# Optimization experiments

Hardware: AMD Instinct MI355X
Metric: run time of the kernel (lower is better)

The kernel has to match this reference:

```python
import jax, jax.numpy as jnp
import numpy as np
from jax import lax

NUM_CLASSES = 80
TOPK = 13
ALPHA = 1.0
BETA = 6.0
EPS = 1e-9
P = 150000
N = 256


def _make_boxes(key, n, scale):
    k1, k2 = jax.random.split(key)
    xy = jax.random.uniform(k1, (n, 2), dtype=jnp.float32) * scale
    wh = jax.random.uniform(k2, (n, 2), dtype=jnp.float32) * (0.2 * scale) + 1.0
    return jnp.concatenate([xy, xy + wh], axis=-1)  # valid x1y1x2y2


def setup_inputs() -> dict:
    key = jax.random.key(0)
    k1, k2, k3, k4 = jax.random.split(key, 4)
    cls_pred = jax.random.uniform(k1, (P, NUM_CLASSES), dtype=jnp.float32)
    bbox_pred = _make_boxes(k2, P, 640.0)
    bbox_gt = _make_boxes(k3, N, 640.0)
    # FG labels are > 0 (code indexes cls_pred[label-1])
    label_gt = jax.random.randint(k4, (N, 1), 1, NUM_CLASSES + 1, dtype=jnp.int32)
    return {"cls_pred": cls_pred, "bbox_pred": bbox_pred, "label_gt": label_gt, "bbox_gt": bbox_gt}


def _ious(bbox1, bbox2, eps=EPS):
    # bbox1: (N,4) gt, bbox2: (P,4) pred -> (N,P)
    b1 = bbox1[:, None, :]
    b2 = bbox2[None, :, :]
    x1y1 = jnp.maximum(b1[..., 0:2], b2[..., 0:2])
    x2y2 = jnp.minimum(b1[..., 2:4], b2[..., 2:4])
    inter = jnp.clip(x2y2 - x1y1, 0.0).prod(-1)
    area1 = jnp.clip(b1[..., 2:4] - b1[..., 0:2], 0.0).prod(-1)
    area2 = jnp.clip(b2[..., 2:4] - b2[..., 0:2], 0.0).prod(-1)
    return inter / (area1 + area2 - inter + eps)


def _metrics_topk(metrics, topk, eps=EPS):
    n, num_priors = metrics.shape
    topk_vals, topk_idxs = lax.top_k(metrics, topk)  # (N,k)
    keep = topk_vals.max(axis=-1, keepdims=True) > eps
    topk_idxs = jnp.where(keep, topk_idxs, 0)
    rows = jnp.arange(n)[:, None]
    counts = jnp.zeros((n, num_priors), jnp.int32).at[rows, topk_idxs].add(1)
    is_in_topk = jnp.where(counts > 1, 0, counts)
    return is_in_topk.astype(metrics.dtype)


def reference(cls_pred, bbox_pred, label_gt, bbox_gt):
    num_priors, num_classes = cls_pred.shape
    n_gt = bbox_gt.shape[0]
    ious = _ious(bbox_gt, bbox_pred)  # (N,P)
    lbl = label_gt.reshape(-1).astype(jnp.int32)  # (N,)
    bbox_cls_scores = jnp.take(cls_pred.T, lbl - 1, axis=0)  # (N,P)
    alignment_metrics = jnp.power(bbox_cls_scores, ALPHA) * jnp.power(ious, BETA)
    mask_positive = _metrics_topk(alignment_metrics, TOPK)  # (N,P) float 0/1
    mask_positive_sum = mask_positive.sum(axis=0)  # (P,)
    # conflict resolution: priors claimed by >1 gt go to the max-iou gt.
    # Applying unconditionally equals the torch data-dependent branch.
    is_max_iou = (jnp.arange(n_gt)[:, None] == ious.argmax(axis=0)[None, :]).astype(ious.dtype)
    mask_positive = jnp.where(mask_positive_sum[None, :] > 1, is_max_iou, mask_positive)
    mask_positive_sum = mask_positive.sum(axis=0)
    assigned_gt_index = mask_positive.argmax(axis=0)  # (P,)
    assigned_labels = lbl[assigned_gt_index]  # (P,)
    assigned_cls = jax.nn.one_hot(assigned_labels - 1, num_classes, dtype=jnp.int32)
    assigned_bboxes = bbox_gt[assigned_gt_index]  # (P,4)
    assigned_labels = jnp.where(mask_positive_sum > 0, assigned_labels, 0)
    return (assigned_gt_index, assigned_labels, assigned_cls, assigned_bboxes)
```

## Files before the change

### kernel.cpp

```cpp
#include <hip/hip_runtime.h>

#define TOPK 13
#define NCLS 80
#define EPSF 1e-9f
#define NSEG 32
#define GPB  8
#define CAP3 512

typedef unsigned long long u64;
typedef float __attribute__((ext_vector_type(4))) f32x4;

__device__ __forceinline__ u64 shfl_xor64(u64 x, int m) {
    int lo = __shfl_xor((int)(unsigned)(x & 0xFFFFFFFFull), m, 64);
    int hi = __shfl_xor((int)(unsigned)(x >> 32), m, 64);
    return ((u64)(unsigned)hi << 32) | (unsigned)lo;
}
__device__ __forceinline__ u64 shfl64(u64 x, int src) {
    int lo = __shfl((int)(unsigned)(x & 0xFFFFFFFFull), src, 64);
    int hi = __shfl((int)(unsigned)(x >> 32), src, 64);
    return ((u64)(unsigned)hi << 32) | (unsigned)lo;
}

__global__ __launch_bounds__(256) void setup(const int* __restrict__ lbl,
                                             int* __restrict__ count,
                                             int* __restrict__ firstg,
                                             int* __restrict__ gorder, int P, int N) {
    int t = threadIdx.x;
    if (blockIdx.x == 0) {
        __shared__ int key[256];
        key[t] = (t < N) ? ((lbl[t] << 8) | t) : 0x7FFFFFFF;
        __syncthreads();
        for (int k = 2; k <= 256; k <<= 1) {
            for (int j = k >> 1; j >= 1; j >>= 1) {
                int ixj = t ^ j;
                if (ixj > t) {
                    int a = key[t], b = key[ixj];
                    bool up = ((t & k) == 0);
                    if (up ? (a > b) : (a < b)) { key[t] = b; key[ixj] = a; }
                }
                __syncthreads();
            }
        }
        if (t < N) gorder[t] = key[t] & 0xFF;
    } else {
        int base = (blockIdx.x - 1) * 1024 + t * 4;
        if (base + 3 < P) {
            *(int4*)&count[base]  = make_int4(0, 0, 0, 0);
            *(int4*)&firstg[base] = make_int4(0x7FFFFFFF, 0x7FFFFFFF, 0x7FFFFFFF, 0x7FFFFFFF);
        } else {
            for (int i = base; i < P; i++) { count[i] = 0; firstg[i] = 0x7FFFFFFF; }
        }
    }
}

__global__ __launch_bounds__(512, 8) void phaseA1(const float* __restrict__ cls,
                                                  const float4* __restrict__ bboxp,
                                                  const float4* __restrict__ bboxg,
                                                  const int* __restrict__ lbl,
                                                  const int* __restrict__ gorder,
                                                  u64* __restrict__ cand,
                                                  int* __restrict__ cnt,
                                                  int P, int N, int seglen) {
#pragma clang fp contract(off)
    const int s = blockIdx.x, tile = blockIdx.y, t = threadIdx.x;
    const int wv = t >> 6, lane = t & 63;
    const int pstart = s * seglen;
    int pend = pstart + seglen; if (pend > P) pend = P;

    __shared__ int pbuf[GPB][CAP3];
    __shared__ int ctr[GPB];

    float4 gb[GPB];
#pragma unroll
    for (int j = 0; j < GPB; j++) {
        int gi8 = tile * GPB + j;
        int gj = (gi8 < N) ? gorder[gi8] : -1;
        gb[j] = (gj >= 0) ? bboxg[gj] : make_float4(0.f, 0.f, 0.f, 0.f);
    }
    if (t < GPB) ctr[t] = 0;
    __syncthreads();

    auto testapp = [&](float4 pb, int p, bool force) {
#pragma unroll
        for (int j = 0; j < GPB; j++) {
            float dx = fminf(gb[j].z, pb.z) - fmaxf(gb[j].x, pb.x);
            float dy = fminf(gb[j].w, pb.w) - fmaxf(gb[j].y, pb.y);
            bool want = ((dx > 0.0f) && (dy > 0.0f)) || force;
            if (want) {
                int slot = atomicAdd(&ctr[j], 1);
                if (slot < CAP3) pbuf[j][slot] = p;
            }
        }
    };

    int p = pstart + t;
    if (p < pend) { testapp(bboxp[p], p, t < 16); p += 512; }
    for (; p + 1536 < pend; p += 2048) {
        float4 pb0 = bboxp[p];
        float4 pb1 = bboxp[p + 512];
        float4 pb2 = bboxp[p + 1024];
        float4 pb3 = bboxp[p + 1536];
        testapp(pb0, p, false);
        testapp(pb1, p + 512, false);
        testapp(pb2, p + 1024, false);
        testapp(pb3, p + 1536, false);
    }
    for (; p < pend; p += 512) testapp(bboxp[p], p, false);
    __syncthreads();

    const int gi8 = tile * GPB + wv;
    if (gi8 >= N) return;
    const int gj = gorder[gi8];
    const float4 gbw = bboxg[gj];
    const float gaw = fmaxf(gbw.z - gbw.x, 0.0f) * fmaxf(gbw.w - gbw.y, 0.0f);
    const int cidx = lbl[gj] - 1;
    const int rawtotal = ctr[wv];
    u64* outp = cand + ((size_t)gj * NSEG + s) * CAP3;

    auto evalk = [&](float4 pb, float sc, int pp) -> u64 {
        float pa = fmaxf(pb.z - pb.x, 0.0f) * fmaxf(pb.w - pb.y, 0.0f);
        float xx1 = fmaxf(gbw.x, pb.x), yy1 = fmaxf(gbw.y, pb.y);
        float xx2 = fminf(gbw.z, pb.z), yy2 = fminf(gbw.w, pb.w);
        float inter = fmaxf(xx2 - xx1, 0.0f) * fmaxf(yy2 - yy1, 0.0f);
        float iou = inter / (((gaw + pa) - inter) + EPSF);
        float i2 = iou * iou;
        float m = sc * ((i2 * i2) * i2);
        unsigned ub = __float_as_uint(m);
        ub ^= ((unsigned)((int)ub >> 31)) | 0x80000000u;
        return ((u64)ub << 32) | (unsigned)(0x7FFFFFFF - pp);
    };

    if (rawtotal <= CAP3) {
        if (lane == 0) cnt[gj * NSEG + s] = rawtotal;
        int e = lane;
        for (; e + 64 < rawtotal; e += 128) {
            int pp0 = pbuf[wv][e];
            int pp1 = pbuf[wv][e + 64];
            float4 pb0 = bboxp[pp0];
            float4 pb1 = bboxp[pp1];
            float sc0 = cls[(size_t)pp0 * NCLS + cidx];
            float sc1 = cls[(size_t)pp1 * NCLS + cidx];
            __builtin_nontemporal_store(evalk(pb0, sc0, pp0), &outp[e]);
            __builtin_nontemporal_store(evalk(pb1, sc1, pp1), &outp[e + 64]);
        }
        for (; e < rawtotal; e += 64) {
            int pp = pbuf[wv][e];
            __builtin_nontemporal_store(
                evalk(bboxp[pp], cls[(size_t)pp * NCLS + cidx], pp), &outp[e]);
        }
    } else {
        u64 K[16];
#pragma unroll
        for (int k = 0; k < 16; k++) K[k] = 0ull;
        auto ins = [&](u64 key) {
            if (key > K[TOPK - 1]) {
#pragma unroll
                for (int k = TOPK - 1; k >= 1; k--) {
                    bool a = key > K[k - 1];
                    K[k] = a ? K[k - 1] : (key > K[k] ? key : K[k]);
                }
                if (key > K[0]) K[0] = key;
            }
        };
        for (int pp = pstart + lane; pp < pend; pp += 64) {
            float4 pb = bboxp[pp];
            float sc = cls[(size_t)pp * NCLS + cidx];
            ins(evalk(pb, sc, pp));
        }
        for (int str = 1; str <= 32; str <<= 1) {
#pragma unroll
            for (int i = 0; i < 8; i++) {
                u64 pa = shfl_xor64(K[15 - i], str);
                u64 pb = shfl_xor64(K[i], str);
                u64 a = K[i], b = K[15 - i];
                K[i]      = (a > pa) ? a : pa;
                K[15 - i] = (b > pb) ? b : pb;
            }
            if (str == 32) break;
#pragma unroll
            for (int j = 8; j >= 1; j >>= 1) {
#pragma unroll
                for (int i = 0; i < 16; i++) {
                    if ((i & j) == 0) {
                        u64 a = K[i], b = K[i | j];
                        K[i] = (a > b) ? a : b;
                        K[i | j] = (a > b) ? b : a;
                    }
                }
            }
        }
        u64 outk = 0ull;
#pragma unroll
        for (int k = 0; k < 16; k++) outk = (lane == k) ? K[k] : outk;
        if (lane < 16) outp[lane] = outk;
        if (lane == 0) cnt[gj * NSEG + s] = 16;
    }
}

__global__ __launch_bounds__(256) void phaseA2(const u64* __restrict__ cand,
                                               const int* __restrict__ cnt,
                                               int* __restrict__ count,
                                               int* __restrict__ firstg) {
    const int g = blockIdx.x;
    const int w = threadIdx.x >> 6, lane = threadIdx.x & 63;
    __shared__ u64 sk[64];

    u64 K[16];
#pragma unroll
    for (int k = 0; k < 16; k++) K[k] = 0ull;

    auto ins = [&](u64 key) {
        if (key > K[TOPK - 1]) {
#pragma unroll
            for (int q = TOPK - 1; q >= 1; q--) {
                bool a = key > K[q - 1];
                K[q] = a ? K[q - 1] : (key > K[q] ? key : K[q]);
            }
            if (key > K[0]) K[0] = key;
        }
    };

    const u64* base = cand + (size_t)g * (NSEG * CAP3);
    const int* cb = cnt + g * NSEG;
    for (int s8 = 0; s8 < NSEG / 4; s8++) {
        int sseg = w * (NSEG / 4) + s8;
        int m = cb[sseg];
        const u64* sp = base + (size_t)sseg * CAP3;
        int e = lane;
        for (; e + 64 < m; e += 128) {
            u64 k0 = sp[e];
            u64 k1 = sp[e + 64];
            ins(k0);
            ins(k1);
        }
        for (; e < m; e += 64) ins(sp[e]);
    }

    for (int str = 1; str <= 32; str <<= 1) {
#pragma unroll
        for (int i = 0; i < 8; i++) {
            u64 pa = shfl_xor64(K[15 - i], str);
            u64 pb = shfl_xor64(K[i], str);
            u64 a = K[i], b = K[15 - i];
            K[i]      = (a > pa) ? a : pa;
            K[15 - i] = (b > pb) ? b : pb;
        }
        if (str == 32) break;
#pragma unroll
        for (int j = 8; j >= 1; j >>= 1) {
#pragma unroll
            for (int i = 0; i < 16; i++) {
                if ((i & j) == 0) {
                    u64 a = K[i], b = K[i | j];
                    K[i] = (a > b) ? a : b;
                    K[i | j] = (a > b) ? b : a;
                }
            }
        }
    }
    u64 outk = 0ull;
#pragma unroll
    for (int k = 0; k < 16; k++) outk = (lane == k) ? K[k] : outk;
    if (lane < 16) sk[w * 16 + lane] = outk;
    __syncthreads();

    if (w == 0) {
        u64 key = sk[lane];
        for (int k = 2; k <= 64; k <<= 1) {
            for (int j = k >> 1; j >= 1; j >>= 1) {
                u64 pk = shfl_xor64(key, j);
                bool lower = (lane & j) == 0;
                bool desc  = (lane & k) == 0;
                bool keepmax = (lower == desc);
                bool pgt = pk > key;
                key = (keepmax == pgt) ? pk : key;
            }
        }
        u64 mx = shfl64(key, 0);
        const unsigned encEpsHi = __float_as_uint(EPSF) | 0x80000000u;
        if (lane < TOPK && (unsigned)(mx >> 32) > encEpsHi) {
            int pi = 0x7FFFFFFF - (int)(unsigned)(key & 0xFFFFFFFFull);
            atomicAdd(&count[pi], 1);
            atomicMin(&firstg[pi], g);
        }
    }
}

__global__ __launch_bounds__(256) void phaseCF(const float4* __restrict__ bboxp,
                                               const float4* __restrict__ bboxg,
                                               const int* __restrict__ lbl,
                                               const int* __restrict__ count,
                                               const int* __restrict__ firstg,
                                               float* __restrict__ out0,
                                               float* __restrict__ out1,
                                               f32x4* __restrict__ outcls4,
                                               float4* __restrict__ outbox4, int P, int N) {
#pragma clang fp contract(off)
    __shared__ float4 gbS[256];
    __shared__ int glS[256];
    __shared__ int clsl[64];
    int t = threadIdx.x;
    if (t < N) { gbS[t] = bboxg[t]; glS[t] = lbl[t]; }
    __syncthreads();
    int p0 = blockIdx.x * 64;
    int nloc = P - p0; if (nloc > 64) nloc = 64;
    if (t < nloc) {
        int p = p0 + t;
        int cnt_ = count[p];
        int gi = 0, pos = 0;
        if (cnt_ == 1) { gi = firstg[p]; pos = 1; }
        else if (cnt_ > 1) {
            float4 pb = bboxp[p];
            float pa = fmaxf(pb.z - pb.x, 0.0f) * fmaxf(pb.w - pb.y, 0.0f);
            float best = -1.0f;
            for (int g = 0; g < N; g++) {
                float4 g4 = gbS[g];
                float gar = fmaxf(g4.z - g4.x, 0.0f) * fmaxf(g4.w - g4.y, 0.0f);
                float xx1 = fmaxf(g4.x, pb.x), yy1 = fmaxf(g4.y, pb.y);
                float xx2 = fminf(g4.z, pb.z), yy2 = fminf(g4.w, pb.w);
                float inter = fmaxf(xx2 - xx1, 0.0f) * fmaxf(yy2 - yy1, 0.0f);
                float iou = inter / (((gar + pa) - inter) + EPSF);
                if (iou > best) { best = iou; gi = g; }
            }
            pos = 1;
        }
        out0[p] = (float)gi;
        out1[p] = pos ? (float)glS[gi] : 0.0f;
        clsl[t] = glS[gi] - 1;
        outbox4[p] = gbS[gi];
    }
    __syncthreads();
    for (int f = t; f < nloc * 20; f += 256) {
        int pl = f / 20, q = f - pl * 20;
        int cl = clsl[pl], c0 = q * 4;
        f32x4 vv = {c0 == cl ? 1.0f : 0.0f, c0 + 1 == cl ? 1.0f : 0.0f,
                    c0 + 2 == cl ? 1.0f : 0.0f, c0 + 3 == cl ? 1.0f : 0.0f};
        __builtin_nontemporal_store(vv, &outcls4[(size_t)p0 * 20 + f]);
    }
}

__global__ __launch_bounds__(256) void phaseC1(const float4* __restrict__ bboxp,
                                               const float4* __restrict__ bboxg,
                                               const int* __restrict__ lbl,
                                               const int* __restrict__ count,
                                               const int* __restrict__ firstg,
                                               float* __restrict__ out0,
                                               float* __restrict__ out1, int P, int N) {
#pragma clang fp contract(off)
    __shared__ float4 gbS[256];
    __shared__ int glS[256];
    if (threadIdx.x < (unsigned)N) {
        gbS[threadIdx.x] = bboxg[threadIdx.x];
        glS[threadIdx.x] = lbl[threadIdx.x];
    }
    __syncthreads();
    int p = blockIdx.x * 256 + threadIdx.x;
    if (p >= P) return;
    int cnt_ = count[p];
    int gi = 0, pos = 0;
    if (cnt_ == 1) { gi = firstg[p]; pos = 1; }
    else if (cnt_ > 1) {
        float4 pb = bboxp[p];
        float pa = fmaxf(pb.z - pb.x, 0.0f) * fmaxf(pb.w - pb.y, 0.0f);
        float best = -1.0f;
        for (int g = 0; g < N; g++) {
            float4 g4 = gbS[g];
            float gar = fmaxf(g4.z - g4.x, 0.0f) * fmaxf(g4.w - g4.y, 0.0f);
            float xx1 = fmaxf(g4.x, pb.x), yy1 = fmaxf(g4.y, pb.y);
            float xx2 = fminf(g4.z, pb.z), yy2 = fminf(g4.w, pb.w);
            float inter = fmaxf(xx2 - xx1, 0.0f) * fmaxf(yy2 - yy1, 0.0f);
            float iou = inter / (((gar + pa) - inter) + EPSF);
            if (iou > best) { best = iou; gi = g; }
        }
        pos = 1;
    }
    out0[p] = (float)gi;
    out1[p] = pos ? (float)glS[gi] : 0.0f;
}

__global__ __launch_bounds__(256) void phaseC2(const float4* __restrict__ bboxg,
                                               const int* __restrict__ lbl,
                                               const float* __restrict__ out0,
                                               float* __restrict__ outcls,
                                               float* __restrict__ outbox, int P, int N) {
    __shared__ float gbb[256 * 4];
    __shared__ int glS[256];
    __shared__ int clsl[256];
    __shared__ int gil[256];
    int tid = threadIdx.x;
    if (tid < N) {
        float4 b = bboxg[tid];
        gbb[tid * 4 + 0] = b.x; gbb[tid * 4 + 1] = b.y;
        gbb[tid * 4 + 2] = b.z; gbb[tid * 4 + 3] = b.w;
        glS[tid] = lbl[tid];
    }
    __syncthreads();
    int p0 = blockIdx.x * 256;
    int nloc = P - p0; if (nloc > 256) nloc = 256;
    if (tid < nloc) {
        int gi = (int)out0[p0 + tid];
        gil[tid] = gi;
        clsl[tid] = glS[gi] - 1;
    }
    __syncthreads();
    for (int f = tid; f < nloc * NCLS; f += 256) {
        int pl = f / NCLS;
        int c  = f - pl * NCLS;
        outcls[(size_t)p0 * NCLS + f] = (c == clsl[pl]) ? 1.0f : 0.0f;
    }
    for (int f = tid; f < nloc * 4; f += 256) {
        int pl = f >> 2, k = f & 3;
        outbox[(size_t)p0 * 4 + f] = gbb[gil[pl] * 4 + k];
    }
}

extern "C" void kernel_launch(void* const* d_in, const int* in_sizes, int n_in,
                              void* d_out, int out_size, void* d_ws, size_t ws_size,
                              hipStream_t stream) {
    const float* cls_pred  = (const float*)d_in[0];
    const float* bbox_pred = (const float*)d_in[1];
    const int*   label_gt  = (const int*)d_in[2];
    const float* bbox_gt   = (const float*)d_in[3];
    int P = in_sizes[1] / 4;
    int N = in_sizes[3] / 4;

    float* out    = (float*)d_out;
    float* out0   = out;
    float* out1   = out + (size_t)P;
    float* outcls = out + (size_t)2 * P;
    float* outbox = out + (size_t)82 * P;

    int pb = (P + 255) / 256;
    int cfb = (P + 63) / 64;
    int seglen = (P + NSEG - 1) / NSEG;
    int gtiles = (N + GPB - 1) / GPB;
    dim3 gridA1(NSEG, gtiles);
    int setupBlocks = 1 + (P + 1023) / 1024;
    size_t candBytes = (size_t)N * NSEG * CAP3 * sizeof(u64);
    size_t cntBytes  = (size_t)N * NSEG * sizeof(int);
    size_t needWs = (size_t)P * 8 + candBytes + cntBytes + (size_t)N * 4 + 64;

    if (ws_size >= needWs) {
        int* count  = (int*)d_ws;
        int* firstg = count + P;
        u64* cand   = (u64*)(firstg + P);
        int* cnt    = (int*)((char*)cand + candBytes);
        int* gorder = cnt + (size_t)N * NSEG;

        setup<<<setupBlocks, 256, 0, stream>>>(label_gt, count, firstg, gorder, P, N);
        phaseA1<<<gridA1, 512, 0, stream>>>(cls_pred, (const float4*)bbox_pred,
                                            (const float4*)bbox_gt, label_gt, gorder,
                                            cand, cnt, P, N, seglen);
        phaseA2<<<N, 256, 0, stream>>>(cand, cnt, count, firstg);
        phaseCF<<<cfb, 256, 0, stream>>>((const float4*)bbox_pred, (const float4*)bbox_gt,
                                         label_gt, count, firstg, out0, out1,
                                         (f32x4*)outcls, (float4*)outbox, P, N);
    } else {
        int* count  = (int*)outbox;
        int* firstg = ((int*)outbox) + P;
        u64* cand   = (u64*)outcls;
        int* cnt    = (int*)((char*)cand + candBytes);
        int* gorder = cnt + (size_t)N * NSEG;

        setup<<<setupBlocks, 256, 0, stream>>>(label_gt, count, firstg, gorder, P, N);
        phaseA1<<<gridA1, 512, 0, stream>>>(cls_pred, (const float4*)bbox_pred,
                                            (const float4*)bbox_gt, label_gt, gorder,
                                            cand, cnt, P, N, seglen);
        phaseA2<<<N, 256, 0, stream>>>(cand, cnt, count, firstg);
        phaseC1<<<pb, 256, 0, stream>>>((const float4*)bbox_pred, (const float4*)bbox_gt,
                                        label_gt, count, firstg, out0, out1, P, N);
        phaseC2<<<pb, 256, 0, stream>>>((const float4*)bbox_gt, label_gt, out0,
                                        outcls, outbox, P, N);
    }
}
```

Before: 219.5 us.

## Fold setup kernel into phaseA1 and simplify phaseCF to one thread per prior

Removes the separate setup launch: every phaseA1 block now redoes the 256-entry bitonic sort of labels in shared memory, and tile-0 blocks zero count/firstg for their own segment. phaseCF drops the shared-memory staging of gt boxes and writes the one-hot rows with one thread per prior. This saves one kernel launch and the gorder round trip, but every block repeats the small sort, and the one-hot writes are now strided per thread rather than coalesced across the block.

```diff
diff --git a/kernel.cpp b/kernel.cpp
--- a/kernel.cpp
+++ b/kernel.cpp
@@ -21,60 +21,56 @@
     return ((u64)(unsigned)hi << 32) | (unsigned)lo;
 }
 
-__global__ __launch_bounds__(256) void setup(const int* __restrict__ lbl,
-                                             int* __restrict__ count,
-                                             int* __restrict__ firstg,
-                                             int* __restrict__ gorder, int P, int N) {
-    int t = threadIdx.x;
-    if (blockIdx.x == 0) {
-        __shared__ int key[256];
-        key[t] = (t < N) ? ((lbl[t] << 8) | t) : 0x7FFFFFFF;
-        __syncthreads();
-        for (int k = 2; k <= 256; k <<= 1) {
-            for (int j = k >> 1; j >= 1; j >>= 1) {
+__global__ __launch_bounds__(512, 8) void phaseA1(const float* __restrict__ cls,
+                                                  const float4* __restrict__ bboxp,
+                                                  const float4* __restrict__ bboxg,
+                                                  const int* __restrict__ lbl,
+                                                  u64* __restrict__ cand,
+                                                  int* __restrict__ cnt,
+                                                  int* __restrict__ count,
+                                                  int* __restrict__ firstg,
+                                                  int P, int N, int seglen) {
+#pragma clang fp contract(off)
+    const int s = blockIdx.x, tile = blockIdx.y, t = threadIdx.x;
+    const int wv = t >> 6, lane = t & 63;
+    const int pstart = s * seglen;
+    int pend = pstart + seglen; if (pend > P) pend = P;
+
+    __shared__ int pbuf[GPB][CAP3];
+    __shared__ int ctr[GPB];
+    __shared__ int gjS[GPB];
+    int* key = &pbuf[0][0];
+
+    if (t < 256) key[t] = (t < N) ? ((lbl[t] << 8) | t) : 0x7FFFFFFF;
+    __syncthreads();
+    for (int k = 2; k <= 256; k <<= 1) {
+        for (int j = k >> 1; j >= 1; j >>= 1) {
+            if (t < 256) {
                 int ixj = t ^ j;
                 if (ixj > t) {
                     int a = key[t], b = key[ixj];
                     bool up = ((t & k) == 0);
                     if (up ? (a > b) : (a < b)) { key[t] = b; key[ixj] = a; }
                 }
-                __syncthreads();
-            }
-        }
-        if (t < N) gorder[t] = key[t] & 0xFF;
-    } else {
-        int base = (blockIdx.x - 1) * 1024 + t * 4;
-        if (base + 3 < P) {
-            *(int4*)&count[base]  = make_int4(0, 0, 0, 0);
-            *(int4*)&firstg[base] = make_int4(0x7FFFFFFF, 0x7FFFFFFF, 0x7FFFFFFF, 0x7FFFFFFF);
-        } else {
-            for (int i = base; i < P; i++) { count[i] = 0; firstg[i] = 0x7FFFFFFF; }
-        }
-    }
-}
-
-__global__ __launch_bounds__(512, 8) void phaseA1(const float* __restrict__ cls,
-                                                  const float4* __restrict__ bboxp,
-                                                  const float4* __restrict__ bboxg,
-                                                  const int* __restrict__ lbl,
-                                                  const int* __restrict__ gorder,
-                                                  u64* __restrict__ cand,
-                                                  int* __restrict__ cnt,
-                                                  int P, int N, int seglen) {
-#pragma clang fp contract(off)
-    const int s = blockIdx.x, tile = blockIdx.y, t = threadIdx.x;
-    const int wv = t >> 6, lane = t & 63;
-    const int pstart = s * seglen;
-    int pend = pstart + seglen; if (pend > P) pend = P;
-
-    __shared__ int pbuf[GPB][CAP3];
-    __shared__ int ctr[GPB];
+            }
+            __syncthreads();
+        }
+    }
+    if (t < GPB) {
+        int gi8 = tile * GPB + t;
+        gjS[t] = (gi8 < N) ? (key[gi8] & 0xFF) : -1;
+    }
+    if (tile == 0) {
+        for (int i = pstart + t; i < pend; i += 512) {
+            count[i] = 0; firstg[i] = 0x7FFFFFFF;
+        }
+    }
+    __syncthreads();
 
     float4 gb[GPB];
 #pragma unroll
     for (int j = 0; j < GPB; j++) {
-        int gi8 = tile * GPB + j;
-        int gj = (gi8 < N) ? gorder[gi8] : -1;
+        int gj = gjS[j];
         gb[j] = (gj >= 0) ? bboxg[gj] : make_float4(0.f, 0.f, 0.f, 0.f);
     }
     if (t < GPB) ctr[t] = 0;
@@ -108,9 +104,8 @@
     for (; p < pend; p += 512) testapp(bboxp[p], p, false);
     __syncthreads();
 
-    const int gi8 = tile * GPB + wv;
-    if (gi8 >= N) return;
-    const int gj = gorder[gi8];
+    const int gj = gjS[wv];
+    if (gj < 0) return;
     const float4 gbw = bboxg[gj];
     const float gaw = fmaxf(gbw.z - gbw.x, 0.0f) * fmaxf(gbw.w - gbw.y, 0.0f);
     const int cidx = lbl[gj] - 1;
@@ -152,14 +147,14 @@
         u64 K[16];
 #pragma unroll
         for (int k = 0; k < 16; k++) K[k] = 0ull;
-        auto ins = [&](u64 key) {
-            if (key > K[TOPK - 1]) {
+        auto ins = [&](u64 key_) {
+            if (key_ > K[TOPK - 1]) {
 #pragma unroll
                 for (int k = TOPK - 1; k >= 1; k--) {
-                    bool a = key > K[k - 1];
-                    K[k] = a ? K[k - 1] : (key > K[k] ? key : K[k]);
+                    bool a = key_ > K[k - 1];
+                    K[k] = a ? K[k - 1] : (key_ > K[k] ? key_ : K[k]);
                 }
-                if (key > K[0]) K[0] = key;
+                if (key_ > K[0]) K[0] = key_;
             }
         };
         for (int pp = pstart + lane; pp < pend; pp += 64) {
@@ -296,46 +291,37 @@
                                                f32x4* __restrict__ outcls4,
                                                float4* __restrict__ outbox4, int P, int N) {
 #pragma clang fp contract(off)
-    __shared__ float4 gbS[256];
-    __shared__ int glS[256];
-    __shared__ int clsl[64];
-    int t = threadIdx.x;
-    if (t < N) { gbS[t] = bboxg[t]; glS[t] = lbl[t]; }
-    __syncthreads();
-    int p0 = blockIdx.x * 64;
-    int nloc = P - p0; if (nloc > 64) nloc = 64;
-    if (t < nloc) {
-        int p = p0 + t;
-        int cnt_ = count[p];
-        int gi = 0, pos = 0;
-        if (cnt_ == 1) { gi = firstg[p]; pos = 1; }
-        else if (cnt_ > 1) {
-            float4 pb = bboxp[p];
-            float pa = fmaxf(pb.z - pb.x, 0.0f) * fmaxf(pb.w - pb.y, 0.0f);
-            float best = -1.0f;
-            for (int g = 0; g < N; g++) {
-                float4 g4 = gbS[g];
-                float gar = fmaxf(g4.z - g4.x, 0.0f) * fmaxf(g4.w - g4.y, 0.0f);
-                float xx1 = fmaxf(g4.x, pb.x), yy1 = fmaxf(g4.y, pb.y);
-                float xx2 = fminf(g4.z, pb.z), yy2 = fminf(g4.w, pb.w);
-                float inter = fmaxf(xx2 - xx1, 0.0f) * fmaxf(yy2 - yy1, 0.0f);
-                float iou = inter / (((gar + pa) - inter) + EPSF);
-                if (iou > best) { best = iou; gi = g; }
-            }
-            pos = 1;
-        }
-        out0[p] = (float)gi;
-        out1[p] = pos ? (float)glS[gi] : 0.0f;
-        clsl[t] = glS[gi] - 1;
-        outbox4[p] = gbS[gi];
-    }
-    __syncthreads();
-    for (int f = t; f < nloc * 20; f += 256) {
-        int pl = f / 20, q = f - pl * 20;
-        int cl = clsl[pl], c0 = q * 4;
+    int p = blockIdx.x * 256 + threadIdx.x;
+    if (p >= P) return;
+    int c = count[p];
+    int gi = 0;
+    if (c == 1) gi = firstg[p];
+    else if (c > 1) {
+        float4 pb = bboxp[p];
+        float pa = fmaxf(pb.z - pb.x, 0.0f) * fmaxf(pb.w - pb.y, 0.0f);
+        float best = -1.0f;
+        for (int g = 0; g < N; g++) {
+            float4 g4 = bboxg[g];
+            float gar = fmaxf(g4.z - g4.x, 0.0f) * fmaxf(g4.w - g4.y, 0.0f);
+            float xx1 = fmaxf(g4.x, pb.x), yy1 = fmaxf(g4.y, pb.y);
+            float xx2 = fminf(g4.z, pb.z), yy2 = fminf(g4.w, pb.w);
+            float inter = fmaxf(xx2 - xx1, 0.0f) * fmaxf(yy2 - yy1, 0.0f);
+            float iou = inter / (((gar + pa) - inter) + EPSF);
+            if (iou > best) { best = iou; gi = g; }
+        }
+    }
+    int lab = lbl[gi];
+    out0[p] = (float)gi;
+    out1[p] = (c > 0) ? (float)lab : 0.0f;
+    outbox4[p] = bboxg[gi];
+    int cl = lab - 1;
+    f32x4* dst = outcls4 + (size_t)p * 20;
+#pragma unroll
+    for (int q = 0; q < 20; q++) {
+        int c0 = q * 4;
         f32x4 vv = {c0 == cl ? 1.0f : 0.0f, c0 + 1 == cl ? 1.0f : 0.0f,
                     c0 + 2 == cl ? 1.0f : 0.0f, c0 + 3 == cl ? 1.0f : 0.0f};
-        __builtin_nontemporal_store(vv, &outcls4[(size_t)p0 * 20 + f]);
+        __builtin_nontemporal_store(vv, dst + q);
     }
 }
 
@@ -431,41 +417,35 @@
     float* outbox = out + (size_t)82 * P;
 
     int pb = (P + 255) / 256;
-    int cfb = (P + 63) / 64;
     int seglen = (P + NSEG - 1) / NSEG;
     int gtiles = (N + GPB - 1) / GPB;
     dim3 gridA1(NSEG, gtiles);
-    int setupBlocks = 1 + (P + 1023) / 1024;
     size_t candBytes = (size_t)N * NSEG * CAP3 * sizeof(u64);
     size_t cntBytes  = (size_t)N * NSEG * sizeof(int);
-    size_t needWs = (size_t)P * 8 + candBytes + cntBytes + (size_t)N * 4 + 64;
+    size_t needWs = (size_t)P * 8 + candBytes + cntBytes + 64;
 
     if (ws_size >= needWs) {
         int* count  = (int*)d_ws;
         int* firstg = count + P;
         u64* cand   = (u64*)(firstg + P);
         int* cnt    = (int*)((char*)cand + candBytes);
-        int* gorder = cnt + (size_t)N * NSEG;
-
-        setup<<<setupBlocks, 256, 0, stream>>>(label_gt, count, firstg, gorder, P, N);
+
         phaseA1<<<gridA1, 512, 0, stream>>>(cls_pred, (const float4*)bbox_pred,
-                                            (const float4*)bbox_gt, label_gt, gorder,
-                                            cand, cnt, P, N, seglen);
+                                            (const float4*)bbox_gt, label_gt,
+                                            cand, cnt, count, firstg, P, N, seglen);
         phaseA2<<<N, 256, 0, stream>>>(cand, cnt, count, firstg);
-        phaseCF<<<cfb, 256, 0, stream>>>((const float4*)bbox_pred, (const float4*)bbox_gt,
-                                         label_gt, count, firstg, out0, out1,
-                                         (f32x4*)outcls, (float4*)outbox, P, N);
+        phaseCF<<<pb, 256, 0, stream>>>((const float4*)bbox_pred, (const float4*)bbox_gt,
+                                        label_gt, count, firstg, out0, out1,
+                                        (f32x4*)outcls, (float4*)outbox, P, N);
     } else {
         int* count  = (int*)outbox;
         int* firstg = ((int*)outbox) + P;
         u64* cand   = (u64*)outcls;
         int* cnt    = (int*)((char*)cand + candBytes);
-        int* gorder = cnt + (size_t)N * NSEG;
-
-        setup<<<setupBlocks, 256, 0, stream>>>(label_gt, count, firstg, gorder, P, N);
+
         phaseA1<<<gridA1, 512, 0, stream>>>(cls_pred, (const float4*)bbox_pred,
-                                            (const float4*)bbox_gt, label_gt, gorder,
-                                            cand, cnt, P, N, seglen);
+                                            (const float4*)bbox_gt, label_gt,
+                                            cand, cnt, count, firstg, P, N, seglen);
         phaseA2<<<N, 256, 0, stream>>>(cand, cnt, count, firstg);
         phaseC1<<<pb, 256, 0, stream>>>((const float4*)bbox_pred, (const float4*)bbox_gt,
                                         label_gt, count, firstg, out0, out1, P, N);
```

Result: slower. 280.4 us (+27.7%).
